# Optimization experiments

Hardware: AMD Instinct MI355X
Metric: run time of the kernel (lower is better)

Reference implementation:

```python
import jax, jax.numpy as jnp
import numpy as np

TOTAL_INSTANCES = 131072
NUM_BAGS = 64
FEATURE_DIM = 512
HIDDEN_DIM = 256


def setup_inputs() -> dict:
    key = jax.random.key(0)
    k1, k2, k3 = jax.random.split(key, 3)
    instance_features = jax.random.normal(k1, (TOTAL_INSTANCES, FEATURE_DIM), dtype=jnp.float32)
    # Equal-sized bags (sum(bag_sizes) == TOTAL_INSTANCES); the reference handles ragged sizes too.
    bag_sizes = jnp.full((NUM_BAGS,), TOTAL_INSTANCES // NUM_BAGS, dtype=jnp.int32)
    W1 = jax.random.normal(k2, (FEATURE_DIM, HIDDEN_DIM), dtype=jnp.float32) * (1.0 / np.sqrt(FEATURE_DIM))
    b1 = jnp.zeros((HIDDEN_DIM,), dtype=jnp.float32)
    W2 = jax.random.normal(k3, (HIDDEN_DIM, 1), dtype=jnp.float32) * (1.0 / np.sqrt(HIDDEN_DIM))
    b2 = jnp.zeros((1,), dtype=jnp.float32)
    return {
        "instance_features": instance_features,
        "bag_sizes": bag_sizes,
        "W1": W1,
        "b1": b1,
        "W2": W2,
        "b2": b2,
    }


def reference(instance_features, bag_sizes, W1, b1, W2, b2):
    # Attention MLP: Linear -> Tanh -> Linear  => scores [T, 1]
    scores = jnp.tanh(instance_features @ W1 + b1) @ W2 + b2
    # Faithful to the original: softmax over dim=0 GLOBALLY across all instances.
    weights = jax.nn.softmax(scores, axis=0)  # [T, 1]
    T = instance_features.shape[0]
    B = bag_sizes.shape[0]
    # Ragged bag membership: instance i belongs to the first bag whose cumulative
    # size exceeds i.
    offsets = jnp.cumsum(bag_sizes)  # [B]
    seg_ids = jnp.searchsorted(offsets, jnp.arange(T), side="right")  # [T]
    # Per-bag weighted sum of instances: [B, feature_dim]
    return jax.ops.segment_sum(instance_features * weights, seg_ids, num_segments=B)
```

## Files before the change

kernel.cpp:

```cpp
#include <hip/hip_runtime.h>

typedef __attribute__((ext_vector_type(8))) short short8;
typedef __attribute__((ext_vector_type(4))) float floatx4;

#define FDIM 512
#define HDIM 256

__device__ __forceinline__ unsigned short f2bf(float f) {
  unsigned int u = __float_as_uint(f);
  u += 0x7fffu + ((u >> 16) & 1u);
  return (unsigned short)(u >> 16);
}

__device__ __forceinline__ short8 pack2(floatx4 a, floatx4 b) {
  short8 r;
  r[0] = (short)f2bf(a[0]); r[1] = (short)f2bf(a[1]);
  r[2] = (short)f2bf(a[2]); r[3] = (short)f2bf(a[3]);
  r[4] = (short)f2bf(b[0]); r[5] = (short)f2bf(b[1]);
  r[6] = (short)f2bf(b[2]); r[7] = (short)f2bf(b[3]);
  return r;
}

__device__ __forceinline__ float fast_tanh(float x) {
  x = fminf(15.0f, fmaxf(-15.0f, x));
  float e = __expf(2.0f * x);
  return (e - 1.0f) / (e + 1.0f);
}

#define GLOAD_A(r0, r1, p)                                                     \
  do {                                                                         \
    asm volatile("global_load_dwordx4 %0, %1, off"                             \
                 : "=v"(r0) : "v"(p) : "memory");                              \
    asm volatile("global_load_dwordx4 %0, %1, off offset:16"                   \
                 : "=v"(r1) : "v"(p) : "memory");                              \
  } while (0)

#define GLOAD_B(r, p)                                                          \
  do {                                                                         \
    asm volatile("global_load_dwordx4 %0, %1, off"                             \
                 : "=v"(r[0]) : "v"(p) : "memory");                            \
    asm volatile("global_load_dwordx4 %0, %1, off offset:256"                  \
                 : "=v"(r[1]) : "v"(p) : "memory");                            \
    asm volatile("global_load_dwordx4 %0, %1, off offset:512"                  \
                 : "=v"(r[2]) : "v"(p) : "memory");                            \
    asm volatile("global_load_dwordx4 %0, %1, off offset:768"                  \
                 : "=v"(r[3]) : "v"(p) : "memory");                            \
  } while (0)

__global__ void __launch_bounds__(256)
k0_pack_w1(const float* __restrict__ W1, unsigned short* __restrict__ W1B,
           float* __restrict__ out) {
  int tid = threadIdx.x;
  int idx = blockIdx.x * 256 + tid;
  if (blockIdx.x < 128) out[blockIdx.x * 256 + tid] = 0.0f;
  int k = idx >> 8;
  int n = idx & 255;
  int s = k >> 5, r = k & 31, oct = r >> 3, e = r & 7;
  W1B[s * 8192 + oct * 2048 + n * 8 + e] = f2bf(W1[idx]);
}

__global__ void __launch_bounds__(256, 2)
k1_scores(const float* __restrict__ X,
          const unsigned short* __restrict__ W1B,
          const float* __restrict__ b1,
          const float* __restrict__ W2,
          float* __restrict__ es,
          float* __restrict__ partials) {
  __shared__ __align__(16) unsigned short As[2][2048];
  __shared__ float scpart[256];

  const int tid  = threadIdx.x;
  const int wn   = tid >> 6;
  const int lane = tid & 63;
  const int l15  = lane & 15;
  const int l4   = lane >> 4;
  const long row0 = (long)blockIdx.x * 64;

  floatx4 acc[4][4];
  #pragma unroll
  for (int m = 0; m < 4; m++)
    #pragma unroll
    for (int n = 0; n < 4; n++)
      acc[m][n] = (floatx4){0.f, 0.f, 0.f, 0.f};

  const int arow = tid >> 2;
  const int aoct = tid & 3;
  const float* xsrc = X + (row0 + arow) * FDIM + aoct * 8;
  const unsigned short* bsrc = W1B + l4 * 2048 + (wn * 64 + l15) * 8;

  floatx4 va0, va1, vb0, vb1;
  short8 br0[4], br1[4];

  GLOAD_A(va0, va1, xsrc);
  GLOAD_B(br0, bsrc);
  GLOAD_A(vb0, vb1, xsrc + 32);

  #pragma unroll
  for (int t = 0; t < 16; ++t) {
    if (t < 15) asm volatile("s_waitcnt vmcnt(6)" ::: "memory");
    else        asm volatile("s_waitcnt vmcnt(4)" ::: "memory");
    __builtin_amdgcn_sched_barrier(0);
    {
      short8 a = ((t & 1) == 0) ? pack2(va0, va1) : pack2(vb0, vb1);
      *(short8*)(&As[t & 1][arow * 32 + aoct * 8]) = a;
    }
    asm volatile("s_waitcnt lgkmcnt(0)" ::: "memory");
    __builtin_amdgcn_sched_barrier(0);
    __builtin_amdgcn_s_barrier();
    if (t < 15) {
      const unsigned short* bp = bsrc + (t + 1) * 8192;
      if (((t + 1) & 1) == 0) GLOAD_B(br0, bp);
      else                    GLOAD_B(br1, bp);
    }
    if (t < 14) {
      const float* pp = xsrc + (t + 2) * 32;
      if ((t & 1) == 0) GLOAD_A(va0, va1, pp);
      else              GLOAD_A(vb0, vb1, pp);
    }
    if (t < 14)       asm volatile("s_waitcnt vmcnt(8)" ::: "memory");
    else if (t == 14) asm volatile("s_waitcnt vmcnt(6)" ::: "memory");
    else              asm volatile("s_waitcnt vmcnt(0)" ::: "memory");
    __builtin_amdgcn_sched_barrier(0);
    short8 af[4];
    #pragma unroll
    for (int m = 0; m < 4; ++m)
      af[m] = *(const short8*)(&As[t & 1][(m * 16 + l15) * 32 + l4 * 8]);
    const short8* bcur = ((t & 1) == 0) ? br0 : br1;
    #pragma unroll
    for (int n = 0; n < 4; ++n)
      #pragma unroll
      for (int m = 0; m < 4; ++m)
        acc[m][n] = __builtin_amdgcn_mfma_f32_16x16x32_bf16(af[m], bcur[n], acc[m][n], 0, 0, 0);
  }

  float rowacc[16];
  #pragma unroll
  for (int i = 0; i < 16; i++) rowacc[i] = 0.f;
  #pragma unroll
  for (int n = 0; n < 4; n++) {
    int c = wn * 64 + n * 16 + l15;
    float b1c = b1[c];
    float w2c = W2[c];
    #pragma unroll
    for (int m = 0; m < 4; m++)
      #pragma unroll
      for (int j = 0; j < 4; j++) {
        float h = fast_tanh(acc[m][n][j] + b1c);
        rowacc[m * 4 + j] = fmaf(h, w2c, rowacc[m * 4 + j]);
      }
  }
  #pragma unroll
  for (int i = 0; i < 16; i++) {
    float v = rowacc[i];
    v += __shfl_xor(v, 1, 64);
    v += __shfl_xor(v, 2, 64);
    v += __shfl_xor(v, 4, 64);
    v += __shfl_xor(v, 8, 64);
    rowacc[i] = v;
  }
  if (l15 == 0) {
    #pragma unroll
    for (int m = 0; m < 4; m++)
      #pragma unroll
      for (int j = 0; j < 4; j++)
        scpart[wn * 64 + m * 16 + l4 * 4 + j] = rowacc[m * 4 + j];
  }
  __syncthreads();

  if (tid < 64) {
    float sv = scpart[0 * 64 + tid] + scpart[1 * 64 + tid] +
               scpart[2 * 64 + tid] + scpart[3 * 64 + tid];
    float ev = __expf(sv);
    es[row0 + tid] = ev;
    float v = ev;
    v += __shfl_xor(v, 1, 64);
    v += __shfl_xor(v, 2, 64);
    v += __shfl_xor(v, 4, 64);
    v += __shfl_xor(v, 8, 64);
    v += __shfl_xor(v, 16, 64);
    v += __shfl_xor(v, 32, 64);
    if (tid == 0) partials[blockIdx.x] = v;
  }
}

__global__ void __launch_bounds__(256)
k2b_finish(const float* __restrict__ partials, int nparts, float* __restrict__ invZ) {
  int tid = threadIdx.x;
  float s = 0.f;
  for (int j = tid; j < nparts; j += 256) s += partials[j];
  #pragma unroll
  for (int m = 1; m < 64; m <<= 1) s += __shfl_xor(s, m, 64);
  __shared__ float wred[4];
  if ((tid & 63) == 0) wred[tid >> 6] = s;
  __syncthreads();
  if (tid == 0) invZ[0] = 1.0f / (wred[0] + wred[1] + wred[2] + wred[3]);
}

__global__ void __launch_bounds__(256)
k3_bagsum(const float* __restrict__ X, const int* __restrict__ bag_sizes,
          const float* __restrict__ es, const float* __restrict__ invZp,
          float* __restrict__ out, int nbags) {
  const int tid = threadIdx.x;
  const int f   = (tid & 127) * 4;
  const int r   = tid >> 7;
  const int bag = blockIdx.x >> 4;
  const int ic  = blockIdx.x & 15;
  int start = 0;
  for (int b = 0; b < bag; ++b) start += bag_sizes[b];
  const int size = bag_sizes[bag];
  const int end = start + size;
  const int chunk = (size + 15) >> 4;
  int i0 = start + ic * chunk;
  int i1 = min(i0 + chunk, end);
  float ax = 0.f, ay = 0.f, az = 0.f, aw = 0.f;
  for (int i = i0 + r; i < i1; i += 2) {
    float w = es[i];
    float4 x = *(const float4*)(X + (size_t)i * FDIM + f);
    ax = fmaf(x.x, w, ax); ay = fmaf(x.y, w, ay);
    az = fmaf(x.z, w, az); aw = fmaf(x.w, w, aw);
  }
  __shared__ float4 red[128];
  if (r == 1) red[tid & 127] = (float4){ax, ay, az, aw};
  __syncthreads();
  if (r == 0) {
    float4 o = red[tid];
    float invZ = invZp[0];
    ax = (ax + o.x) * invZ; ay = (ay + o.y) * invZ;
    az = (az + o.z) * invZ; aw = (aw + o.w) * invZ;
    float* op = out + (size_t)bag * FDIM + f;
    atomicAdd(op + 0, ax); atomicAdd(op + 1, ay);
    atomicAdd(op + 2, az); atomicAdd(op + 3, aw);
  }
}

extern "C" void kernel_launch(void* const* d_in, const int* in_sizes, int n_in,
                              void* d_out, int out_size, void* d_ws, size_t ws_size,
                              hipStream_t stream) {
  const float* X         = (const float*)d_in[0];
  const int*   bag_sizes = (const int*)d_in[1];
  const float* W1        = (const float*)d_in[2];
  const float* b1        = (const float*)d_in[3];
  const float* W2        = (const float*)d_in[4];
  float* out = (float*)d_out;

  const int T     = in_sizes[0] / FDIM;
  const int nbags = in_sizes[1];
  const int nblk  = T / 64;

  char* ws = (char*)d_ws;
  unsigned short* W1B = (unsigned short*)ws;
  float* es       = (float*)(ws + 262144);
  float* partials = (float*)(ws + 262144 + 524288);
  float* invZ     = (float*)(ws + 262144 + 524288 + 8192);

  hipLaunchKernelGGL(k0_pack_w1, dim3(512), dim3(256), 0, stream, W1, W1B, out);
  hipLaunchKernelGGL(k1_scores, dim3(nblk), dim3(256), 0, stream,
                     X, W1B, b1, W2, es, partials);
  hipLaunchKernelGGL(k2b_finish, dim3(1), dim3(256), 0, stream, partials, nblk, invZ);
  hipLaunchKernelGGL(k3_bagsum, dim3(nbags * 16), dim3(256), 0, stream,
                     X, bag_sizes, es, invZ, out, nbags);
}
```

Before: 107.1 us.

## Write bf16 copy of X in score kernel and bag-sum from it

The score kernel now stores the bf16-packed X tiles it already builds for the MFMA to a workspace buffer. A new bag-sum kernel reads this half-size copy instead of the fp32 input, and it computes the softmax normaliser itself, so the separate finish kernel is no longer launched. This halves the second read of X but adds a 128 MB write. The weighted bag sums also become bf16-accurate, and the path needs a large workspace, falling back to the old pipeline otherwise.

```diff
diff --git a/kernel.cpp b/kernel.cpp
--- a/kernel.cpp
+++ b/kernel.cpp
@@ -10,6 +10,10 @@
   unsigned int u = __float_as_uint(f);
   u += 0x7fffu + ((u >> 16) & 1u);
   return (unsigned short)(u >> 16);
+}
+
+__device__ __forceinline__ float bf2f(unsigned short u) {
+  return __uint_as_float(((unsigned int)u) << 16);
 }
 
 __device__ __forceinline__ short8 pack2(floatx4 a, floatx4 b) {
@@ -26,6 +30,8 @@
   float e = __expf(2.0f * x);
   return (e - 1.0f) / (e + 1.0f);
 }
+
+#define VM(n) asm volatile("s_waitcnt vmcnt(" #n ")" ::: "memory")
 
 #define GLOAD_A(r0, r1, p)                                                     \
   do {                                                                         \
@@ -59,11 +65,13 @@
   W1B[s * 8192 + oct * 2048 + n * 8 + e] = f2bf(W1[idx]);
 }
 
+template <bool WX>
 __global__ void __launch_bounds__(256, 2)
 k1_scores(const float* __restrict__ X,
           const unsigned short* __restrict__ W1B,
           const float* __restrict__ b1,
           const float* __restrict__ W2,
+          unsigned short* __restrict__ Xb,
           float* __restrict__ es,
           float* __restrict__ partials) {
   __shared__ __align__(16) unsigned short As[2][2048];
@@ -86,10 +94,12 @@
   const int arow = tid >> 2;
   const int aoct = tid & 3;
   const float* xsrc = X + (row0 + arow) * FDIM + aoct * 8;
+  unsigned short* xbdst = Xb + (row0 + arow) * FDIM + aoct * 8;
   const unsigned short* bsrc = W1B + l4 * 2048 + (wn * 64 + l15) * 8;
 
   floatx4 va0, va1, vb0, vb1;
   short8 br0[4], br1[4];
+  short8 a0s = {0,0,0,0,0,0,0,0}, a1s = {0,0,0,0,0,0,0,0};
 
   GLOAD_A(va0, va1, xsrc);
   GLOAD_B(br0, bsrc);
@@ -97,12 +107,29 @@
 
   #pragma unroll
   for (int t = 0; t < 16; ++t) {
-    if (t < 15) asm volatile("s_waitcnt vmcnt(6)" ::: "memory");
-    else        asm volatile("s_waitcnt vmcnt(4)" ::: "memory");
+    if constexpr (WX) {
+      if (t == 0)      VM(6);
+      else if (t < 15) VM(7);
+      else             VM(5);
+    } else {
+      if (t < 15) VM(6);
+      else        VM(4);
+    }
     __builtin_amdgcn_sched_barrier(0);
     {
-      short8 a = ((t & 1) == 0) ? pack2(va0, va1) : pack2(vb0, vb1);
-      *(short8*)(&As[t & 1][arow * 32 + aoct * 8]) = a;
+      if ((t & 1) == 0) {
+        a0s = pack2(va0, va1);
+        *(short8*)(&As[0][arow * 32 + aoct * 8]) = a0s;
+        if constexpr (WX)
+          asm volatile("global_store_dwordx4 %0, %1, off"
+                       :: "v"(xbdst + t * 32), "v"(a0s) : "memory");
+      } else {
+        a1s = pack2(vb0, vb1);
+        *(short8*)(&As[1][arow * 32 + aoct * 8]) = a1s;
+        if constexpr (WX)
+          asm volatile("global_store_dwordx4 %0, %1, off"
+                       :: "v"(xbdst + t * 32), "v"(a1s) : "memory");
+      }
     }
     asm volatile("s_waitcnt lgkmcnt(0)" ::: "memory");
     __builtin_amdgcn_sched_barrier(0);
@@ -117,10 +144,17 @@
       if ((t & 1) == 0) GLOAD_A(va0, va1, pp);
       else              GLOAD_A(vb0, vb1, pp);
     }
-    if (t < 14)       asm volatile("s_waitcnt vmcnt(8)" ::: "memory");
-    else if (t == 14) asm volatile("s_waitcnt vmcnt(6)" ::: "memory");
-    else              asm volatile("s_waitcnt vmcnt(0)" ::: "memory");
+    if constexpr (WX) {
+      if (t < 14)       VM(9);
+      else if (t == 14) VM(7);
+      else              VM(1);
+    } else {
+      if (t < 14)       VM(8);
+      else if (t == 14) VM(6);
+      else              VM(0);
+    }
     __builtin_amdgcn_sched_barrier(0);
+    if constexpr (WX) asm volatile("" :: "v"(a0s), "v"(a1s));
     short8 af[4];
     #pragma unroll
     for (int m = 0; m < 4; ++m)
@@ -131,6 +165,10 @@
       #pragma unroll
       for (int m = 0; m < 4; ++m)
         acc[m][n] = __builtin_amdgcn_mfma_f32_16x16x32_bf16(af[m], bcur[n], acc[m][n], 0, 0, 0);
+  }
+  if constexpr (WX) {
+    asm volatile("" :: "v"(a0s), "v"(a1s));
+    VM(0);
   }
 
   float rowacc[16];
@@ -180,6 +218,63 @@
     v += __shfl_xor(v, 16, 64);
     v += __shfl_xor(v, 32, 64);
     if (tid == 0) partials[blockIdx.x] = v;
+  }
+}
+
+__global__ void __launch_bounds__(256)
+k3_bagsum_bf16(const unsigned short* __restrict__ Xb,
+               const int* __restrict__ bag_sizes,
+               const float* __restrict__ es,
+               const float* __restrict__ partials, int nparts,
+               float* __restrict__ out, int nbags) {
+  __shared__ float pacc[3][512];
+  __shared__ float invZ_s;
+  const int tid = threadIdx.x;
+  const int fc  = tid & 63;
+  const int par = tid >> 6;
+
+  if (par == 3) {
+    float s = 0.f;
+    for (int j = fc; j < nparts; j += 64) s += partials[j];
+    #pragma unroll
+    for (int m = 1; m < 64; m <<= 1) s += __shfl_xor(s, m, 64);
+    if (fc == 0) invZ_s = 1.0f / s;
+  }
+
+  const int bag = blockIdx.x >> 4;
+  const int ic  = blockIdx.x & 15;
+  int start = 0;
+  for (int b = 0; b < bag; ++b) start += bag_sizes[b];
+  const int size = bag_sizes[bag];
+  const int end = start + size;
+  const int chunk = (size + 15) >> 4;
+  int i0 = start + ic * chunk;
+  int i1 = min(i0 + chunk, end);
+
+  float a[8];
+  #pragma unroll
+  for (int e = 0; e < 8; ++e) a[e] = 0.f;
+  for (int i = i0 + par; i < i1; i += 4) {
+    float w = es[i];
+    short8 xv = *(const short8*)(Xb + (size_t)i * FDIM + fc * 8);
+    #pragma unroll
+    for (int e = 0; e < 8; ++e)
+      a[e] = fmaf(bf2f((unsigned short)xv[e]), w, a[e]);
+  }
+  if (par != 0) {
+    #pragma unroll
+    for (int e = 0; e < 8; ++e) pacc[par - 1][fc * 8 + e] = a[e];
+  }
+  __syncthreads();
+  if (par == 0) {
+    float invZ = invZ_s;
+    float* op = out + (size_t)bag * FDIM + fc * 8;
+    #pragma unroll
+    for (int e = 0; e < 8; ++e) {
+      float tot = a[e] + pacc[0][fc * 8 + e] + pacc[1][fc * 8 + e] +
+                  pacc[2][fc * 8 + e];
+      atomicAdd(op + e, tot * invZ);
+    }
   }
 }
 
@@ -252,11 +347,20 @@
   float* es       = (float*)(ws + 262144);
   float* partials = (float*)(ws + 262144 + 524288);
   float* invZ     = (float*)(ws + 262144 + 524288 + 8192);
+  unsigned short* Xb = (unsigned short*)(ws + 1048576);
+  const size_t NEED = 1048576 + (size_t)T * FDIM * 2;
 
   hipLaunchKernelGGL(k0_pack_w1, dim3(512), dim3(256), 0, stream, W1, W1B, out);
-  hipLaunchKernelGGL(k1_scores, dim3(nblk), dim3(256), 0, stream,
-                     X, W1B, b1, W2, es, partials);
-  hipLaunchKernelGGL(k2b_finish, dim3(1), dim3(256), 0, stream, partials, nblk, invZ);
-  hipLaunchKernelGGL(k3_bagsum, dim3(nbags * 16), dim3(256), 0, stream,
-                     X, bag_sizes, es, invZ, out, nbags);
-}
+  if (ws_size >= NEED) {
+    hipLaunchKernelGGL(k1_scores<true>, dim3(nblk), dim3(256), 0, stream,
+                       X, W1B, b1, W2, Xb, es, partials);
+    hipLaunchKernelGGL(k3_bagsum_bf16, dim3(nbags * 16), dim3(256), 0, stream,
+                       Xb, bag_sizes, es, partials, nblk, out, nbags);
+  } else {
+    hipLaunchKernelGGL(k1_scores<false>, dim3(nblk), dim3(256), 0, stream,
+                       X, W1B, b1, W2, Xb, es, partials);
+    hipLaunchKernelGGL(k2b_finish, dim3(1), dim3(256), 0, stream, partials, nblk, invZ);
+    hipLaunchKernelGGL(k3_bagsum, dim3(nbags * 16), dim3(256), 0, stream,
+                       X, bag_sizes, es, invZ, out, nbags);
+  }
+}
```

Result: slower. 147.8 us (+37.9%).

## Fuse weighted bag-sum into score kernel using register-held bf16 X tiles

Applied to the files above, without the earlier changes.

The score kernel keeps each thread's packed bf16 slices of X in registers and, once the per-row exp scores are known, computes per-bag weighted partial sums in shared memory. Each block writes up to two per-bag partial vectors (atomics for any further segments). A new per-bag reduce kernel sums these partials and applies the global 1/Z normalisation. This removes the second full pass over X (256 MB) and the separate invZ kernel, at the cost of more registers (16 short8 per thread), larger shared memory, and a weighted sum taken from bf16-rounded X instead of fp32, which lowers accuracy. The fused path runs only when the workspace is large enough.

```diff
diff --git a/kernel.cpp b/kernel.cpp
--- a/kernel.cpp
+++ b/kernel.cpp
@@ -49,25 +49,36 @@
 
 __global__ void __launch_bounds__(256)
 k0_pack_w1(const float* __restrict__ W1, unsigned short* __restrict__ W1B,
-           float* __restrict__ out) {
+           float* __restrict__ out, float* __restrict__ outAcc) {
   int tid = threadIdx.x;
   int idx = blockIdx.x * 256 + tid;
-  if (blockIdx.x < 128) out[blockIdx.x * 256 + tid] = 0.0f;
+  if (blockIdx.x < 128) {
+    out[blockIdx.x * 256 + tid] = 0.0f;
+    if (outAcc) outAcc[blockIdx.x * 256 + tid] = 0.0f;
+  }
   int k = idx >> 8;
   int n = idx & 255;
   int s = k >> 5, r = k & 31, oct = r >> 3, e = r & 7;
   W1B[s * 8192 + oct * 2048 + n * 8 + e] = f2bf(W1[idx]);
 }
 
+template <bool FUSE>
 __global__ void __launch_bounds__(256, 2)
 k1_scores(const float* __restrict__ X,
           const unsigned short* __restrict__ W1B,
           const float* __restrict__ b1,
           const float* __restrict__ W2,
           float* __restrict__ es,
-          float* __restrict__ partials) {
-  __shared__ __align__(16) unsigned short As[2][2048];
-  __shared__ float scpart[256];
+          float* __restrict__ partials,
+          float* __restrict__ partial_out,
+          int* __restrict__ bagid,
+          float* __restrict__ outAcc,
+          const int* __restrict__ bag_sizes,
+          int nbags) {
+  __shared__ __align__(16) unsigned char smem[FUSE ? 33024 : 9472];
+  unsigned short (*As)[2048] = (unsigned short(*)[2048])smem;
+  float* scpart = (float*)(smem + 8192);
+  float* es_s   = (float*)(smem + (FUSE ? 32768 : 9216));
 
   const int tid  = threadIdx.x;
   const int wn   = tid >> 6;
@@ -90,6 +101,7 @@
 
   floatx4 va0, va1, vb0, vb1;
   short8 br0[4], br1[4];
+  short8 xa[16];
 
   GLOAD_A(va0, va1, xsrc);
   GLOAD_B(br0, bsrc);
@@ -103,6 +115,7 @@
     {
       short8 a = ((t & 1) == 0) ? pack2(va0, va1) : pack2(vb0, vb1);
       *(short8*)(&As[t & 1][arow * 32 + aoct * 8]) = a;
+      if constexpr (FUSE) xa[t] = a;
     }
     asm volatile("s_waitcnt lgkmcnt(0)" ::: "memory");
     __builtin_amdgcn_sched_barrier(0);
@@ -171,7 +184,8 @@
     float sv = scpart[0 * 64 + tid] + scpart[1 * 64 + tid] +
                scpart[2 * 64 + tid] + scpart[3 * 64 + tid];
     float ev = __expf(sv);
-    es[row0 + tid] = ev;
+    es_s[tid] = ev;
+    if constexpr (!FUSE) es[row0 + tid] = ev;
     float v = ev;
     v += __shfl_xor(v, 1, 64);
     v += __shfl_xor(v, 2, 64);
@@ -181,6 +195,128 @@
     v += __shfl_xor(v, 32, 64);
     if (tid == 0) partials[blockIdx.x] = v;
   }
+  __syncthreads();
+
+  if constexpr (FUSE) {
+    float* pacc = (float*)smem;
+    const int g = wn * 4 + (lane >> 4);
+    const bool wr = ((lane & 12) == 0);
+
+    int bag = 0; long cum = 0;
+    while (bag + 1 < nbags && cum + (long)bag_sizes[bag] <= row0) {
+      cum += bag_sizes[bag]; ++bag;
+    }
+    long bagEnd = cum + (long)bag_sizes[bag];
+
+    int segidx = 0;
+    int rs = 0;
+    while (rs < 64) {
+      int se = (int)(bagEnd - row0 < 64 ? bagEnd - row0 : 64);
+      if (se < rs) se = rs;
+      float wme = (arow >= rs && arow < se) ? es_s[arow] : 0.f;
+      #pragma unroll
+      for (int t = 0; t < 16; ++t) {
+        const unsigned int* ui = (const unsigned int*)&xa[t];
+        float p[8];
+        #pragma unroll
+        for (int d = 0; d < 4; ++d) {
+          p[2 * d]     = __uint_as_float(ui[d] << 16) * wme;
+          p[2 * d + 1] = __uint_as_float(ui[d] & 0xffff0000u) * wme;
+        }
+        #pragma unroll
+        for (int e = 0; e < 8; ++e) {
+          p[e] += __shfl_xor(p[e], 4, 64);
+          p[e] += __shfl_xor(p[e], 8, 64);
+        }
+        if (wr) {
+          float* dst = &pacc[g * 512 + t * 32 + aoct * 8];
+          *(float4*)dst       = (float4){p[0], p[1], p[2], p[3]};
+          *(float4*)(dst + 4) = (float4){p[4], p[5], p[6], p[7]};
+        }
+      }
+      __syncthreads();
+      {
+        int f = tid * 2;
+        float tx = 0.f, ty = 0.f;
+        #pragma unroll
+        for (int gg = 0; gg < 16; ++gg) {
+          float2 v = *(const float2*)&pacc[gg * 512 + f];
+          tx += v.x; ty += v.y;
+        }
+        long blk = blockIdx.x;
+        if (segidx == 0) {
+          *(float2*)&partial_out[(blk * 2 + 0) * 512 + f] = (float2){tx, ty};
+          if (tid == 0) bagid[blk * 2 + 0] = bag;
+        } else if (segidx == 1) {
+          *(float2*)&partial_out[(blk * 2 + 1) * 512 + f] = (float2){tx, ty};
+          if (tid == 0) bagid[blk * 2 + 1] = bag;
+        } else {
+          atomicAdd(&outAcc[(long)bag * 512 + f],     tx);
+          atomicAdd(&outAcc[(long)bag * 512 + f + 1], ty);
+        }
+      }
+      __syncthreads();
+      ++segidx;
+      rs = se;
+      if (rs < 64) {
+        ++bag;
+        if (bag >= nbags) { bagEnd = row0 + 64; bag = nbags - 1; }
+        else bagEnd += (long)bag_sizes[bag];
+      }
+    }
+    if (segidx < 2) {
+      int f = tid * 2;
+      *(float2*)&partial_out[((long)blockIdx.x * 2 + 1) * 512 + f] =
+          (float2){0.f, 0.f};
+      if (tid == 0) bagid[blockIdx.x * 2 + 1] = -1;
+    }
+  }
+}
+
+__global__ void __launch_bounds__(256)
+k2_reduce(const int* __restrict__ bag_sizes, int nbags,
+          const float* __restrict__ partials, int nblk,
+          const int* __restrict__ bagid,
+          const float* __restrict__ partial_out,
+          const float* __restrict__ outAcc,
+          float* __restrict__ out) {
+  __shared__ float wred[4];
+  __shared__ float invZ_s;
+  const int tid = threadIdx.x;
+  const int bag = blockIdx.x;
+
+  float s = 0.f;
+  for (int j = tid; j < nblk; j += 256) s += partials[j];
+  #pragma unroll
+  for (int m = 1; m < 64; m <<= 1) s += __shfl_xor(s, m, 64);
+  if ((tid & 63) == 0) wred[tid >> 6] = s;
+  __syncthreads();
+  if (tid == 0) invZ_s = 1.0f / (wred[0] + wred[1] + wred[2] + wred[3]);
+  __syncthreads();
+  const float invZ = invZ_s;
+
+  long off = 0;
+  for (int b = 0; b < bag; ++b) off += bag_sizes[b];
+  const int size = bag_sizes[bag];
+
+  const int f = tid * 2;
+  float tx = outAcc[(long)bag * 512 + f];
+  float ty = outAcc[(long)bag * 512 + f + 1];
+  if (size > 0) {
+    int b0 = (int)(off >> 6);
+    int b1 = (int)((off + size - 1) >> 6);
+    for (int blk = b0; blk <= b1; ++blk) {
+      #pragma unroll
+      for (int slot = 0; slot < 2; ++slot) {
+        if (bagid[blk * 2 + slot] == bag) {
+          float2 v = *(const float2*)&partial_out[((long)blk * 2 + slot) * 512 + f];
+          tx += v.x; ty += v.y;
+        }
+      }
+    }
+  }
+  out[(long)bag * 512 + f]     = tx * invZ;
+  out[(long)bag * 512 + f + 1] = ty * invZ;
 }
 
 __global__ void __launch_bounds__(256)
@@ -249,14 +385,33 @@
 
   char* ws = (char*)d_ws;
   unsigned short* W1B = (unsigned short*)ws;
-  float* es       = (float*)(ws + 262144);
-  float* partials = (float*)(ws + 262144 + 524288);
-  float* invZ     = (float*)(ws + 262144 + 524288 + 8192);
-
-  hipLaunchKernelGGL(k0_pack_w1, dim3(512), dim3(256), 0, stream, W1, W1B, out);
-  hipLaunchKernelGGL(k1_scores, dim3(nblk), dim3(256), 0, stream,
-                     X, W1B, b1, W2, es, partials);
-  hipLaunchKernelGGL(k2b_finish, dim3(1), dim3(256), 0, stream, partials, nblk, invZ);
-  hipLaunchKernelGGL(k3_bagsum, dim3(nbags * 16), dim3(256), 0, stream,
-                     X, bag_sizes, es, invZ, out, nbags);
-}
+  float* partials  = (float*)(ws + 262144);
+  float* es        = (float*)(ws + 270336);
+  float* invZ      = (float*)(ws + 794624);
+  int*   bagid     = (int*)(ws + 1048576);
+  float* outAcc    = (float*)(ws + 1064960);
+  float* partial_out = (float*)(ws + 1196032);
+  const size_t NEED = 1196032 + (size_t)nblk * 2 * 512 * 4;
+
+  const bool fuse = (ws_size >= NEED);
+
+  hipLaunchKernelGGL(k0_pack_w1, dim3(512), dim3(256), 0, stream,
+                     W1, W1B, out, fuse ? outAcc : (float*)nullptr);
+  if (fuse) {
+    hipLaunchKernelGGL(k1_scores<true>, dim3(nblk), dim3(256), 0, stream,
+                       X, W1B, b1, W2, es, partials,
+                       partial_out, bagid, outAcc, bag_sizes, nbags);
+    hipLaunchKernelGGL(k2_reduce, dim3(nbags), dim3(256), 0, stream,
+                       bag_sizes, nbags, partials, nblk,
+                       bagid, partial_out, outAcc, out);
+  } else {
+    hipLaunchKernelGGL(k1_scores<false>, dim3(nblk), dim3(256), 0, stream,
+                       X, W1B, b1, W2, es, partials,
+                       (float*)nullptr, (int*)nullptr, (float*)nullptr,
+                       bag_sizes, nbags);
+    hipLaunchKernelGGL(k2b_finish, dim3(1), dim3(256), 0, stream,
+                       partials, nblk, invZ);
+    hipLaunchKernelGGL(k3_bagsum, dim3(nbags * 16), dim3(256), 0, stream,
+                       X, bag_sizes, es, invZ, out, nbags);
+  }
+}
```

New measurement: 135.6 us. 1.27x slower.
